# Optimization experiments

Hardware: AMD Instinct MI355X
Metric: run time of the kernel (lower is better)

The kernel has to match this reference:

```python
import jax, jax.numpy as jnp
import numpy as np

C_M = 256
C = 32
C_Z = 128
EPS = 1e-5


def setup_inputs() -> dict:
    key = jax.random.key(0)
    ks = jax.random.split(key, 8)
    b, s, i = 1, 128, 256
    msa = jax.random.normal(ks[0], (b, s, i, C_M), dtype=jnp.float32)
    scale_in = 1.0 / np.sqrt(C_M)
    scale_out = 1.0 / np.sqrt(C * C)
    return {
        "msa_representation": msa,
        "ln_w": jnp.ones((C_M,), jnp.float32),
        "ln_b": jnp.zeros((C_M,), jnp.float32),
        "w_left": jax.random.normal(ks[1], (C_M, C), jnp.float32) * scale_in,
        "b_left": jax.random.normal(ks[2], (C,), jnp.float32) * scale_in,
        "w_right": jax.random.normal(ks[3], (C_M, C), jnp.float32) * scale_in,
        "b_right": jax.random.normal(ks[4], (C,), jnp.float32) * scale_in,
        "w_out": jax.random.normal(ks[5], (C * C, C_Z), jnp.float32) * scale_out,
        "b_out": jax.random.normal(ks[6], (C_Z,), jnp.float32) * scale_out,
    }


def reference(msa_representation, ln_w, ln_b, w_left, b_left, w_right, b_right, w_out, b_out):
    x = msa_representation
    # LayerNorm over c_m
    mu = jnp.mean(x, axis=-1, keepdims=True)
    var = jnp.mean(jnp.square(x - mu), axis=-1, keepdims=True)
    x = (x - mu) * jax.lax.rsqrt(var + EPS) * ln_w + ln_b
    # dual projections: [b, s, i, c]
    A = x @ w_left + b_left
    B = x @ w_right + b_right
    s_dim = x.shape[1]
    # outer product mean over MSA depth s: [b, i, j, c, c]
    outer = jnp.einsum('bsic,bsjd->bijcd', A, B) / s_dim
    b_, i_, j_ = outer.shape[0], outer.shape[1], outer.shape[2]
    flat = outer.reshape(b_, i_, j_, C * C)
    return flat @ w_out + b_out
```

## Files before the change

kernel.cpp:

```cpp
#include <hip/hip_runtime.h>

typedef __attribute__((ext_vector_type(8))) short short8;
typedef __attribute__((ext_vector_type(4))) float f32x4;

#define CM 256
#define CC 32
#define CZ 128
#define SDIM 128
#define IDIM 256

__device__ __forceinline__ unsigned short f2bf(float f) {
  union { float f; unsigned u; } v; v.f = f;
  unsigned r = v.u + 0x7fffu + ((v.u >> 16) & 1u);
  return (unsigned short)(r >> 16);
}
__device__ __forceinline__ unsigned pack_bf2(float a, float b) {
  union { float f; unsigned u; } x, y; x.f = a; y.f = b;
  return ((x.u + 0x8000u) >> 16) | ((y.u + 0x8000u) & 0xffff0000u);
}

__global__ void k_prep(const float* __restrict__ wl, const float* __restrict__ wr,
                       const float* __restrict__ wo,
                       unsigned short* __restrict__ wlrT2, unsigned short* __restrict__ WF) {
  int t = blockIdx.x * 256 + threadIdx.x;
  if (t < 2048) {
    int frag = t >> 6, lane = t & 63;
    int nt = frag >> 3, ks = frag & 7;
    int ln = lane & 15, qd = lane >> 4;
    int c64 = nt * 16 + ln;
#pragma unroll
    for (int e = 0; e < 8; ++e) {
      int cm = ks * 32 + qd * 8 + e;
      float v = (c64 < CC) ? wl[cm * CC + c64] : wr[cm * CC + (c64 - CC)];
      wlrT2[(size_t)t * 8 + e] = f2bf(v);
    }
  } else {
    int t2 = t - 2048;
    if (t2 < 8 * 32 * 64) {
      int zt = t2 >> 11, ks = (t2 >> 6) & 31, lane = t2 & 63;
      int ln = lane & 15, qd = lane >> 4;
      int z = zt * 16 + ln;
#pragma unroll
      for (int e = 0; e < 8; ++e) {
        int c = qd * 8 + e, d = ks;
        WF[(size_t)t2 * 8 + e] = f2bf(wo[(c * 32 + d) * CZ + z] * (1.0f / 128.0f));
      }
    }
  }
}

__global__ __launch_bounds__(256) void k_lnproj(
    const float* __restrict__ x, const float* __restrict__ lnw, const float* __restrict__ lnb,
    const float* __restrict__ bl, const float* __restrict__ br,
    const unsigned short* __restrict__ wlrT2,
    unsigned short* __restrict__ A2, unsigned short* __restrict__ Bbuf) {
  __shared__ __align__(16) unsigned short xn[64][264];
  __shared__ __align__(16) unsigned short sT[64][72];
  int tid = threadIdx.x;
  int lane = tid & 63, ww = tid >> 6;
  int qd = lane >> 4, ln = lane & 15;
  int i = blockIdx.x, sh = blockIdx.y;

  for (int rr = 0; rr < 16; ++rr) {
    int sl = ww * 16 + rr;
    int s = sh * 64 + sl;
    float4 v = ((const float4*)(x + ((size_t)s * IDIM + i) * CM))[lane];
    float s1 = v.x + v.y + v.z + v.w;
    float s2 = v.x * v.x + v.y * v.y + v.z * v.z + v.w * v.w;
#pragma unroll
    for (int off = 32; off; off >>= 1) {
      s1 += __shfl_xor(s1, off);
      s2 += __shfl_xor(s2, off);
    }
    float mu = s1 * (1.0f / 256.0f);
    float var = s2 * (1.0f / 256.0f) - mu * mu;
    float rs = rsqrtf(var + 1e-5f);
    float4 w4 = ((const float4*)lnw)[lane];
    float4 b4 = ((const float4*)lnb)[lane];
    ushort4 h;
    h.x = f2bf((v.x - mu) * rs * w4.x + b4.x);
    h.y = f2bf((v.y - mu) * rs * w4.y + b4.y);
    h.z = f2bf((v.z - mu) * rs * w4.z + b4.z);
    h.w = f2bf((v.w - mu) * rs * w4.w + b4.w);
    *(ushort4*)&xn[sl][lane * 4] = h;
  }
  __syncthreads();

  f32x4 acc[4];
#pragma unroll
  for (int nt = 0; nt < 4; ++nt) acc[nt] = (f32x4){0.f, 0.f, 0.f, 0.f};
#pragma unroll
  for (int ks = 0; ks < 8; ++ks) {
    short8 af = *(const short8*)&xn[ww * 16 + ln][ks * 32 + qd * 8];
#pragma unroll
    for (int nt = 0; nt < 4; ++nt) {
      short8 bf = *(const short8*)(wlrT2 + ((size_t)((nt * 8 + ks) * 64 + lane)) * 8);
      acc[nt] = __builtin_amdgcn_mfma_f32_16x16x32_bf16(af, bf, acc[nt], 0, 0, 0);
    }
  }
#pragma unroll
  for (int nt = 0; nt < 4; ++nt) {
    int c64 = nt * 16 + ln;
    float bias = (c64 < CC) ? bl[c64] : br[c64 - CC];
    ushort4 h;
    h.x = f2bf(acc[nt][0] + bias);
    h.y = f2bf(acc[nt][1] + bias);
    h.z = f2bf(acc[nt][2] + bias);
    h.w = f2bf(acc[nt][3] + bias);
    *(ushort4*)&sT[c64][ww * 16 + qd * 4] = h;
  }
  __syncthreads();

  {
    int rtloc = ww >> 1, ksl = ww & 1;
    short8 v = *(const short8*)&sT[rtloc * 16 + ln][ksl * 32 + qd * 8];
    *(short8*)(A2 + ((size_t)(((2 * i + rtloc) * 4 + (sh * 2 + ksl)) * 64 + lane)) * 8) = v;
  }
  {
    int row = tid >> 3, ch = tid & 7;
    short8 v = *(const short8*)&sT[CC + row][ch * 8];
    *(short8*)(Bbuf + ((size_t)(i * CC + row)) * SDIM + sh * 64 + ch * 8) = v;
  }
}

__global__ __launch_bounds__(512, 4) void k_main(
    const unsigned short* __restrict__ A2, const unsigned short* __restrict__ Bbuf,
    const unsigned short* __restrict__ WF, const float* __restrict__ bout,
    float* __restrict__ out) {
  extern __shared__ __align__(16) char lds[];
  unsigned short* sB = (unsigned short*)lds;
  unsigned short* sP = (unsigned short*)lds;
  float* redR = (float*)lds;
  int tid = threadIdx.x;
  int lane = tid & 63, ww = tid >> 6;
  int qd = lane >> 4, ln = lane & 15;
  int i0 = blockIdx.x * 8, j0 = blockIdx.y * 4;

#pragma unroll
  for (int t = 0; t < 4; ++t) {
    int idx = tid + t * 512;
    int r = idx >> 4, ch = idx & 15;
    short8 v = *(const short8*)(Bbuf + (size_t)(j0 * CC + r) * SDIM + ch * 8);
    *(short8*)&sB[r * 136 + ch * 8] = v;
  }
  __syncthreads();

  int wy = ww >> 1, wx = ww & 1;
  f32x4 acc1[4][4];
#pragma unroll
  for (int a = 0; a < 4; ++a)
#pragma unroll
    for (int b = 0; b < 4; ++b) acc1[a][b] = (f32x4){0.f, 0.f, 0.f, 0.f};
#pragma unroll
  for (int ks = 0; ks < 4; ++ks) {
    short8 af[4];
#pragma unroll
    for (int ti = 0; ti < 4; ++ti)
      af[ti] = *(const short8*)(A2 + ((size_t)((i0 * 2 + wy * 4 + ti) * 4 + ks) * 64 + lane) * 8);
#pragma unroll
    for (int tj = 0; tj < 4; ++tj) {
      short8 bf = *(const short8*)&sB[(wx * 64 + tj * 16 + ln) * 136 + ks * 32 + qd * 8];
#pragma unroll
      for (int ti = 0; ti < 4; ++ti)
        acc1[ti][tj] = __builtin_amdgcn_mfma_f32_16x16x32_bf16(af[ti], bf, acc1[ti][tj], 0, 0, 0);
    }
  }
  __syncthreads();

#pragma unroll
  for (int ti = 0; ti < 4; ++ti) {
    int iloc = wy * 2 + (ti >> 1);
    int cbase = 16 * (ti & 1) + qd * 4;
    int cb = cbase >> 3;
#pragma unroll
    for (int tj = 0; tj < 4; ++tj) {
      int jloc = wx * 2 + (tj >> 1);
      int d = 16 * (tj & 1) + ln;
      int p = iloc * 4 + jloc;
      uint2 u;
      u.x = pack_bf2(acc1[ti][tj][0], acc1[ti][tj][1]);
      u.y = pack_bf2(acc1[ti][tj][2], acc1[ti][tj][3]);
      *(uint2*)&sP[p * 1032 + d * 32 + ((((d >> 1) & 3) ^ cb) * 8) + (cbase & 7)] = u;
    }
  }
  __syncthreads();

  int ztp = ww & 3, kq = ww >> 2;
  f32x4 acc2[2][2];
#pragma unroll
  for (int a = 0; a < 2; ++a)
#pragma unroll
    for (int b = 0; b < 2; ++b) acc2[a][b] = (f32x4){0.f, 0.f, 0.f, 0.f};
#pragma unroll
  for (int cc = 0; cc < 16; ++cc) {
    int ks = kq * 16 + cc;
    short8 afr[2];
#pragma unroll
    for (int mt = 0; mt < 2; ++mt)
      afr[mt] = *(const short8*)&sP[(mt * 16 + ln) * 1032 + ks * 32 + ((((ks >> 1) & 3) ^ qd) * 8)];
#pragma unroll
    for (int h2 = 0; h2 < 2; ++h2) {
      int zt = ztp * 2 + h2;
      short8 bfr = *(const short8*)(WF + ((size_t)(zt * 32 + ks) * 64 + lane) * 8);
#pragma unroll
      for (int mt = 0; mt < 2; ++mt)
        acc2[h2][mt] = __builtin_amdgcn_mfma_f32_16x16x32_bf16(bfr, afr[mt], acc2[h2][mt], 0, 0, 0);
    }
  }

  __syncthreads();
  if (kq == 1) {
#pragma unroll
    for (int h2 = 0; h2 < 2; ++h2)
#pragma unroll
      for (int mt = 0; mt < 2; ++mt)
        *(f32x4*)&redR[(((ztp * 2 + h2) * 2 + mt) << 8) + lane * 4] = acc2[h2][mt];
  }
  __syncthreads();
  if (kq == 0) {
#pragma unroll
    for (int h2 = 0; h2 < 2; ++h2) {
      int z = (ztp * 2 + h2) * 16 + qd * 4;
      f32x4 bz = *(const f32x4*)(bout + z);
#pragma unroll
      for (int mt = 0; mt < 2; ++mt) {
        int p = mt * 16 + ln;
        f32x4 v = acc2[h2][mt] +
                  *(const f32x4*)&redR[(((ztp * 2 + h2) * 2 + mt) << 8) + lane * 4] + bz;
        int i = i0 + (p >> 2), j = j0 + (p & 3);
        *(f32x4*)&out[((size_t)i * IDIM + j) * CZ + z] = v;
      }
    }
  }
}

extern "C" void kernel_launch(void* const* d_in, const int* in_sizes, int n_in,
                              void* d_out, int out_size, void* d_ws, size_t ws_size,
                              hipStream_t stream) {
  const float* msa = (const float*)d_in[0];
  const float* lnw = (const float*)d_in[1];
  const float* lnb = (const float*)d_in[2];
  const float* wl  = (const float*)d_in[3];
  const float* bl  = (const float*)d_in[4];
  const float* wr  = (const float*)d_in[5];
  const float* br  = (const float*)d_in[6];
  const float* wo  = (const float*)d_in[7];
  const float* bo  = (const float*)d_in[8];
  float* out = (float*)d_out;

  char* ws = (char*)d_ws;
  unsigned short* A2    = (unsigned short*)ws;
  unsigned short* Bbuf  = (unsigned short*)(ws + (2u << 20));
  unsigned short* wlrT2 = (unsigned short*)(ws + (4u << 20));
  unsigned short* WF    = (unsigned short*)(ws + (4u << 20) + 32768);

  (void)hipFuncSetAttribute((const void*)k_main,
                            hipFuncAttributeMaxDynamicSharedMemorySize, 66048);

  k_prep<<<72, 256, 0, stream>>>(wl, wr, wo, wlrT2, WF);
  k_lnproj<<<dim3(256, 2), 256, 0, stream>>>(msa, lnw, lnb, bl, br, wlrT2, A2, Bbuf);
  k_main<<<dim3(32, 64), 512, 66048, stream>>>(A2, Bbuf, WF, bo, out);
}
```

Before: 145.1 us.

## Make k_main persistent over j tiles with register-resident A and prefetched B

k_main now runs 256 blocks, each covering one 8-row i tile and looping over four 8-column j tiles. The block's A fragments stay in registers across the whole loop, and the next B tile is prefetched into registers while the second GEMM runs. The j tile per iteration doubles, so the second GEMM processes 64 pairs and each WF fragment load feeds more MFMAs. Block indices are swizzled, and LDS per block grows to 160KB, which caps occupancy at one 512-thread block per CU. More registers are live, and the launch bound drops to 2.

```diff
diff --git a/kernel.cpp b/kernel.cpp
--- a/kernel.cpp
+++ b/kernel.cpp
@@ -123,112 +123,144 @@
   }
 }
 
-__global__ __launch_bounds__(512, 4) void k_main(
+__global__ __launch_bounds__(512, 2) void k_main(
     const unsigned short* __restrict__ A2, const unsigned short* __restrict__ Bbuf,
     const unsigned short* __restrict__ WF, const float* __restrict__ bout,
     float* __restrict__ out) {
   extern __shared__ __align__(16) char lds[];
-  unsigned short* sB = (unsigned short*)lds;
   unsigned short* sP = (unsigned short*)lds;
+  unsigned short* sB = (unsigned short*)(lds + 94208);
   float* redR = (float*)lds;
   int tid = threadIdx.x;
   int lane = tid & 63, ww = tid >> 6;
   int qd = lane >> 4, ln = lane & 15;
-  int i0 = blockIdx.x * 8, j0 = blockIdx.y * 4;
-
-#pragma unroll
+  int bx = blockIdx.x;
+  int itile = (bx & 7) * 4 + ((bx >> 3) & 3);
+  int jg = bx >> 5;
+  int i0 = itile * 8;
+  int wy = ww >> 1, wx = ww & 1;
+  int ztp = ww & 3, kq = ww >> 2;
+
+  short8 afA[16];
+  short8 bpre[8];
+
+#pragma unroll
+  for (int tt = 0; tt < 8; ++tt) {
+    int idx = tid + tt * 512;
+    int r = idx >> 4, ch = idx & 15;
+    bpre[tt] = *(const short8*)(Bbuf + ((size_t)(jg * 4) * 256 + r) * SDIM + ch * 8);
+  }
+#pragma unroll
+  for (int ti = 0; ti < 4; ++ti)
+#pragma unroll
+    for (int ks = 0; ks < 4; ++ks)
+      afA[ti * 4 + ks] =
+          *(const short8*)(A2 + ((size_t)((i0 * 2 + wy * 4 + ti) * 4 + ks) * 64 + lane) * 8);
+
   for (int t = 0; t < 4; ++t) {
-    int idx = tid + t * 512;
-    int r = idx >> 4, ch = idx & 15;
-    short8 v = *(const short8*)(Bbuf + (size_t)(j0 * CC + r) * SDIM + ch * 8);
-    *(short8*)&sB[r * 136 + ch * 8] = v;
-  }
-  __syncthreads();
-
-  int wy = ww >> 1, wx = ww & 1;
-  f32x4 acc1[4][4];
-#pragma unroll
-  for (int a = 0; a < 4; ++a)
-#pragma unroll
-    for (int b = 0; b < 4; ++b) acc1[a][b] = (f32x4){0.f, 0.f, 0.f, 0.f};
-#pragma unroll
-  for (int ks = 0; ks < 4; ++ks) {
-    short8 af[4];
-#pragma unroll
-    for (int ti = 0; ti < 4; ++ti)
-      af[ti] = *(const short8*)(A2 + ((size_t)((i0 * 2 + wy * 4 + ti) * 4 + ks) * 64 + lane) * 8);
-#pragma unroll
-    for (int tj = 0; tj < 4; ++tj) {
-      short8 bf = *(const short8*)&sB[(wx * 64 + tj * 16 + ln) * 136 + ks * 32 + qd * 8];
-#pragma unroll
-      for (int ti = 0; ti < 4; ++ti)
-        acc1[ti][tj] = __builtin_amdgcn_mfma_f32_16x16x32_bf16(af[ti], bf, acc1[ti][tj], 0, 0, 0);
-    }
-  }
-  __syncthreads();
-
-#pragma unroll
-  for (int ti = 0; ti < 4; ++ti) {
-    int iloc = wy * 2 + (ti >> 1);
-    int cbase = 16 * (ti & 1) + qd * 4;
-    int cb = cbase >> 3;
-#pragma unroll
-    for (int tj = 0; tj < 4; ++tj) {
-      int jloc = wx * 2 + (tj >> 1);
-      int d = 16 * (tj & 1) + ln;
-      int p = iloc * 4 + jloc;
-      uint2 u;
-      u.x = pack_bf2(acc1[ti][tj][0], acc1[ti][tj][1]);
-      u.y = pack_bf2(acc1[ti][tj][2], acc1[ti][tj][3]);
-      *(uint2*)&sP[p * 1032 + d * 32 + ((((d >> 1) & 3) ^ cb) * 8) + (cbase & 7)] = u;
-    }
-  }
-  __syncthreads();
-
-  int ztp = ww & 3, kq = ww >> 2;
-  f32x4 acc2[2][2];
-#pragma unroll
-  for (int a = 0; a < 2; ++a)
-#pragma unroll
-    for (int b = 0; b < 2; ++b) acc2[a][b] = (f32x4){0.f, 0.f, 0.f, 0.f};
-#pragma unroll
-  for (int cc = 0; cc < 16; ++cc) {
-    int ks = kq * 16 + cc;
-    short8 afr[2];
-#pragma unroll
-    for (int mt = 0; mt < 2; ++mt)
-      afr[mt] = *(const short8*)&sP[(mt * 16 + ln) * 1032 + ks * 32 + ((((ks >> 1) & 3) ^ qd) * 8)];
-#pragma unroll
-    for (int h2 = 0; h2 < 2; ++h2) {
-      int zt = ztp * 2 + h2;
-      short8 bfr = *(const short8*)(WF + ((size_t)(zt * 32 + ks) * 64 + lane) * 8);
-#pragma unroll
-      for (int mt = 0; mt < 2; ++mt)
-        acc2[h2][mt] = __builtin_amdgcn_mfma_f32_16x16x32_bf16(bfr, afr[mt], acc2[h2][mt], 0, 0, 0);
-    }
-  }
-
-  __syncthreads();
-  if (kq == 1) {
-#pragma unroll
-    for (int h2 = 0; h2 < 2; ++h2)
-#pragma unroll
-      for (int mt = 0; mt < 2; ++mt)
-        *(f32x4*)&redR[(((ztp * 2 + h2) * 2 + mt) << 8) + lane * 4] = acc2[h2][mt];
-  }
-  __syncthreads();
-  if (kq == 0) {
-#pragma unroll
-    for (int h2 = 0; h2 < 2; ++h2) {
-      int z = (ztp * 2 + h2) * 16 + qd * 4;
-      f32x4 bz = *(const f32x4*)(bout + z);
-#pragma unroll
-      for (int mt = 0; mt < 2; ++mt) {
-        int p = mt * 16 + ln;
-        f32x4 v = acc2[h2][mt] +
-                  *(const f32x4*)&redR[(((ztp * 2 + h2) * 2 + mt) << 8) + lane * 4] + bz;
-        int i = i0 + (p >> 2), j = j0 + (p & 3);
-        *(f32x4*)&out[((size_t)i * IDIM + j) * CZ + z] = v;
+    int j0 = (jg * 4 + t) * 8;
+
+#pragma unroll
+    for (int tt = 0; tt < 8; ++tt) {
+      int idx = tid + tt * 512;
+      int r = idx >> 4, ch = idx & 15;
+      *(short8*)&sB[r * 136 + ch * 8] = bpre[tt];
+    }
+    __syncthreads();
+
+#pragma unroll
+    for (int h = 0; h < 2; ++h) {
+      int wxx = h * 2 + wx;
+      f32x4 acc1[4][4];
+#pragma unroll
+      for (int a = 0; a < 4; ++a)
+#pragma unroll
+        for (int b = 0; b < 4; ++b) acc1[a][b] = (f32x4){0.f, 0.f, 0.f, 0.f};
+#pragma unroll
+      for (int ks = 0; ks < 4; ++ks)
+#pragma unroll
+        for (int tj = 0; tj < 4; ++tj) {
+          short8 bf = *(const short8*)&sB[((wxx * 4 + tj) * 16 + ln) * 136 + ks * 32 + qd * 8];
+#pragma unroll
+          for (int ti = 0; ti < 4; ++ti)
+            acc1[ti][tj] =
+                __builtin_amdgcn_mfma_f32_16x16x32_bf16(afA[ti * 4 + ks], bf, acc1[ti][tj], 0, 0, 0);
+        }
+      if (h == 1) __syncthreads();
+#pragma unroll
+      for (int ti = 0; ti < 4; ++ti) {
+        int iloc = wy * 2 + (ti >> 1);
+        int cbase = 16 * (ti & 1) + qd * 4;
+        int cb = cbase >> 3;
+#pragma unroll
+        for (int tj = 0; tj < 4; ++tj) {
+          int jl2 = wx * 2 + (tj >> 1);
+          int d = 16 * (tj & 1) + ln;
+          int p = h * 32 + iloc * 4 + jl2;
+          uint2 u;
+          u.x = pack_bf2(acc1[ti][tj][0], acc1[ti][tj][1]);
+          u.y = pack_bf2(acc1[ti][tj][2], acc1[ti][tj][3]);
+          *(uint2*)&sP[p * 1032 + d * 32 + ((((d >> 1) & 3) ^ cb) * 8) + (cbase & 7)] = u;
+        }
+      }
+    }
+    __syncthreads();
+
+    if (t < 3) {
+#pragma unroll
+      for (int tt = 0; tt < 8; ++tt) {
+        int idx = tid + tt * 512;
+        int r = idx >> 4, ch = idx & 15;
+        bpre[tt] = *(const short8*)(Bbuf + ((size_t)(jg * 4 + t + 1) * 256 + r) * SDIM + ch * 8);
+      }
+    }
+
+    f32x4 acc2[2][4];
+#pragma unroll
+    for (int a = 0; a < 2; ++a)
+#pragma unroll
+      for (int b = 0; b < 4; ++b) acc2[a][b] = (f32x4){0.f, 0.f, 0.f, 0.f};
+#pragma unroll
+    for (int cc = 0; cc < 16; ++cc) {
+      int ks = kq * 16 + cc;
+      short8 afr[4];
+#pragma unroll
+      for (int mt = 0; mt < 4; ++mt)
+        afr[mt] =
+            *(const short8*)&sP[(mt * 16 + ln) * 1032 + ks * 32 + ((((ks >> 1) & 3) ^ qd) * 8)];
+#pragma unroll
+      for (int h2 = 0; h2 < 2; ++h2) {
+        int zt = ztp * 2 + h2;
+        short8 bfr = *(const short8*)(WF + ((size_t)(zt * 32 + ks) * 64 + lane) * 8);
+#pragma unroll
+        for (int mt = 0; mt < 4; ++mt)
+          acc2[h2][mt] =
+              __builtin_amdgcn_mfma_f32_16x16x32_bf16(bfr, afr[mt], acc2[h2][mt], 0, 0, 0);
+      }
+    }
+    __syncthreads();
+
+    if (kq == 1) {
+#pragma unroll
+      for (int h2 = 0; h2 < 2; ++h2)
+#pragma unroll
+        for (int mt = 0; mt < 4; ++mt)
+          *(f32x4*)&redR[(((ztp * 2 + h2) * 4 + mt) << 8) + lane * 4] = acc2[h2][mt];
+    }
+    __syncthreads();
+    if (kq == 0) {
+#pragma unroll
+      for (int h2 = 0; h2 < 2; ++h2) {
+        int z = (ztp * 2 + h2) * 16 + qd * 4;
+        f32x4 bz = *(const f32x4*)(bout + z);
+#pragma unroll
+        for (int mt = 0; mt < 4; ++mt) {
+          int p = mt * 16 + ln;
+          f32x4 v = acc2[h2][mt] +
+                    *(const f32x4*)&redR[(((ztp * 2 + h2) * 4 + mt) << 8) + lane * 4] + bz;
+          int i = i0 + ((p >> 2) & 7), j = j0 + (p >> 5) * 4 + (p & 3);
+          *(f32x4*)&out[((size_t)i * IDIM + j) * CZ + z] = v;
+        }
       }
     }
   }
@@ -255,9 +287,9 @@
   unsigned short* WF    = (unsigned short*)(ws + (4u << 20) + 32768);
 
   (void)hipFuncSetAttribute((const void*)k_main,
-                            hipFuncAttributeMaxDynamicSharedMemorySize, 66048);
+                            hipFuncAttributeMaxDynamicSharedMemorySize, 163840);
 
   k_prep<<<72, 256, 0, stream>>>(wl, wr, wo, wlrT2, WF);
   k_lnproj<<<dim3(256, 2), 256, 0, stream>>>(msa, lnw, lnb, bl, br, wlrT2, A2, Bbuf);
-  k_main<<<dim3(32, 64), 512, 66048, stream>>>(A2, Bbuf, WF, bo, out);
-}
+  k_main<<<256, 512, 163840, stream>>>(A2, Bbuf, WF, bo, out);
+}
```

Result: slower. 193.6 us (+33.4%).
